# Kernel tuning notes

Measured on AMD Instinct MI355X. Metric: run time of the kernel, lower is better.

Reference implementation:

```python
import jax, jax.numpy as jnp
import numpy as np

HEAD_SIZE = 64


def setup_inputs() -> dict:
    key = jax.random.key(0)
    ks = jax.random.split(key, 6)
    B, S, D, H = 8, 2048, 1024, HEAD_SIZE
    return {
        "q": jax.random.normal(ks[0], (B, S, D), dtype=jnp.float32),
        "k": jax.random.normal(ks[1], (B, S, D), dtype=jnp.float32),
        "v": jax.random.normal(ks[2], (B, S, D), dtype=jnp.float32),
        "mask": jnp.ones((B, S), dtype=bool),
        "Wq": jax.random.normal(ks[3], (D, H), dtype=jnp.float32) * (D ** -0.5),
        "Wk": jax.random.normal(ks[4], (D, H), dtype=jnp.float32) * (D ** -0.5),
        "Wv": jax.random.normal(ks[5], (D, H), dtype=jnp.float32) * (D ** -0.5),
    }


def reference(q, k, v, mask, Wq, Wk, Wv):
    # Linear projections (bias=False): x @ W, W is [n_embd, head_size]
    qp = jnp.einsum("bsd,dh->bsh", q, Wq)
    kp = jnp.einsum("bsd,dh->bsh", k, Wk)
    vp = jnp.einsum("bsd,dh->bsh", v, Wv)
    scale = HEAD_SIZE ** -0.5
    scores = jnp.einsum("bqh,bkh->bqk", qp, kp) * scale  # [B, Sq, Sk]
    # 2-D mask [B, Sk] -> broadcast over query dim (mask.unsqueeze(1))
    scores = jnp.where(mask[:, None, :], scores, -jnp.inf)
    attn = jax.nn.softmax(scores, axis=-1)
    # dropout is identity in eval mode (deterministic reference)
    out = jnp.einsum("bqk,bkh->bqh", attn, vp)
    return out
```

## Files before the change

### kernel.cpp

```cpp
#include <hip/hip_runtime.h>
#include <hip/hip_bf16.h>
#include <math.h>

#define B_ 8
#define S_ 2048
#define D_ 1024
#define H_ 64
#define M_ (B_*S_)
#define SPLIT 4
#define KEYS_PER_SPLIT (S_/SPLIT)

typedef __attribute__((ext_vector_type(8))) short bf16x8;
typedef __attribute__((ext_vector_type(8))) unsigned short u16x8;
typedef __attribute__((ext_vector_type(4))) float f32x4;

__device__ inline unsigned short f2bf(float f) {
    unsigned int u = __builtin_bit_cast(unsigned int, f);
    u += 0x7fffu + ((u >> 16) & 1u);
    return (unsigned short)(u >> 16);
}

__global__ __launch_bounds__(256) void mask_kernel(const unsigned char* __restrict__ mask,
                                                   float* __restrict__ mmul, int n) {
    int j = blockIdx.x * 256 + threadIdx.x;
    if (j >= n) return;
    bool boolLayout = mask[1] != 0;
    int mv = boolLayout ? (int)mask[j] : ((const int*)mask)[j];
    mmul[j] = mv ? 1.0f : 0.0f;
}

__global__ __launch_bounds__(256) void wprep_kernel(
    const float* __restrict__ Wq, const float* __restrict__ Wk, const float* __restrict__ Wv,
    unsigned short* __restrict__ Wt)
{
    const int m = blockIdx.y;
    const float* W = (m == 0) ? Wq : (m == 1) ? Wk : Wv;
    unsigned short* Wo = Wt + (size_t)m * 64 * 1024;
    __shared__ unsigned short T[64][65];
    const int t = threadIdx.x;
    const int k0 = blockIdx.x * 64;
    #pragma unroll
    for (int i = 0; i < 16; i++) {
        int vi = t + i * 256;
        int kk = vi >> 6, n = vi & 63;
        T[kk][n] = f2bf(W[(size_t)(k0 + kk) * 64 + n]);
    }
    __syncthreads();
    #pragma unroll
    for (int i = 0; i < 4; i++) {
        int vi = t + i * 256;
        int n = vi >> 4, k4 = vi & 15;
        ushort4 u;
        u.x = T[k4*4+0][n]; u.y = T[k4*4+1][n]; u.z = T[k4*4+2][n]; u.w = T[k4*4+3][n];
        *(ushort4*)&Wo[(size_t)n * 1024 + k0 + k4*4] = u;
    }
}

__global__ __launch_bounds__(256) void proj_kernel(
    const float* __restrict__ q, const float* __restrict__ kx, const float* __restrict__ vx,
    const unsigned short* __restrict__ Wt,
    unsigned short* __restrict__ qp, unsigned short* __restrict__ kp, unsigned short* __restrict__ vp)
{
    const int m = blockIdx.y;
    const float* x = (m == 0) ? q : (m == 1) ? kx : vx;
    const unsigned short* Wm = Wt + (size_t)m * 64 * 1024;
    unsigned short* outp = (m == 0) ? qp : (m == 1) ? kp : vp;

    const int t = threadIdx.x;
    const int w = t >> 6, l = t & 63;
    const int lrow = l & 15, quad = l >> 4;
    const size_t arow = (size_t)(blockIdx.x * 64 + w * 16 + lrow);
    const float* xr = x + arow * D_ + quad * 8;
    const unsigned short* wb = Wm + lrow * 1024 + quad * 8;

    f32x4 acc[4] = {};
    #pragma unroll 1
    for (int ks = 0; ks < D_; ks += 128) {
        float4 xa[8];
        bf16x8 wf[4][4];
        #pragma unroll
        for (int kk = 0; kk < 4; kk++) {
            xa[2*kk]   = *(const float4*)(xr + ks + kk*32);
            xa[2*kk+1] = *(const float4*)(xr + ks + kk*32 + 4);
        }
        #pragma unroll
        for (int kk = 0; kk < 4; kk++)
            #pragma unroll
            for (int c = 0; c < 4; c++)
                wf[kk][c] = *(const bf16x8*)(wb + ks + kk*32 + c * 16 * 1024);
        __builtin_amdgcn_sched_barrier(0);
        #pragma unroll
        for (int kk = 0; kk < 4; kk++) {
            bf16x8 af;
            af[0] = (short)f2bf(xa[2*kk].x); af[1] = (short)f2bf(xa[2*kk].y);
            af[2] = (short)f2bf(xa[2*kk].z); af[3] = (short)f2bf(xa[2*kk].w);
            af[4] = (short)f2bf(xa[2*kk+1].x); af[5] = (short)f2bf(xa[2*kk+1].y);
            af[6] = (short)f2bf(xa[2*kk+1].z); af[7] = (short)f2bf(xa[2*kk+1].w);
            #pragma unroll
            for (int c = 0; c < 4; c++)
                acc[c] = __builtin_amdgcn_mfma_f32_16x16x32_bf16(af, wf[kk][c], acc[c], 0, 0, 0);
        }
    }
    const float sc = (m == 0) ? 0.125f : 1.0f;
    const int orow = blockIdx.x * 64 + w * 16 + quad * 4;
    #pragma unroll
    for (int c = 0; c < 4; c++)
        #pragma unroll
        for (int r = 0; r < 4; r++)
            outp[(size_t)(orow + r) * H_ + c * 16 + lrow] = f2bf(acc[c][r] * sc);
}

__global__ __launch_bounds__(256) void attn_kernel(
    const unsigned short* __restrict__ qp, const unsigned short* __restrict__ kp,
    const unsigned short* __restrict__ vp, const float* __restrict__ mmul,
    float* __restrict__ po, float* __restrict__ pl)
{
    __shared__ unsigned short Qs[64][72];
    __shared__ unsigned short Ks[64][72];
    __shared__ unsigned short Vt[64][72];
    __shared__ unsigned short Ps[64][72];

    const int t = threadIdx.x;
    const int w = t >> 6, l = t & 63;
    const int lrow = l & 15, lq = l >> 4;
    const int lk8 = lq * 8;
    const int b = blockIdx.y, q0 = blockIdx.x * 64;
    const int split = blockIdx.z;
    const int key0 = split * KEYS_PER_SPLIT;
    const size_t basebs = (size_t)b * S_;

    const int srow = t >> 3, sc8 = t & 7;

    #pragma unroll
    for (int i = 0; i < 2; i++) {
        u16x8 u = *(const u16x8*)&qp[(basebs + q0 + srow + i*32) * H_ + sc8 * 8];
        *(u16x8*)&Qs[srow + i*32][sc8 * 8] = u;
    }

    u16x8 kr[2], vr[2];
    #pragma unroll
    for (int i = 0; i < 2; i++) {
        kr[i] = *(const u16x8*)&kp[(basebs + key0 + srow + i*32) * H_ + sc8 * 8];
        vr[i] = *(const u16x8*)&vp[(basebs + key0 + srow + i*32) * H_ + sc8 * 8];
    }

    float lsum[4] = {0.f, 0.f, 0.f, 0.f};
    f32x4 o[4] = {};

    for (int kt = 0; kt < KEYS_PER_SPLIT / 64; kt++) {
        __syncthreads();
        #pragma unroll
        for (int i = 0; i < 2; i++) {
            *(u16x8*)&Ks[srow + i*32][sc8 * 8] = kr[i];
            #pragma unroll
            for (int j = 0; j < 8; j++)
                Vt[sc8*8 + j][(srow + i*32) ^ (sc8*8)] = vr[i][j];
        }
        __syncthreads();
        if (kt + 1 < KEYS_PER_SPLIT / 64) {
            const int k0n = key0 + (kt + 1) * 64;
            #pragma unroll
            for (int i = 0; i < 2; i++) {
                kr[i] = *(const u16x8*)&kp[(basebs + k0n + srow + i*32) * H_ + sc8 * 8];
                vr[i] = *(const u16x8*)&vp[(basebs + k0n + srow + i*32) * H_ + sc8 * 8];
            }
        }
        const int k0 = key0 + kt * 64;
        float mm[4];
        #pragma unroll
        for (int c = 0; c < 4; c++) mm[c] = mmul[basebs + k0 + c*16 + lrow];

        f32x4 s[4] = {};
        #pragma unroll
        for (int kk = 0; kk < 2; kk++) {
            bf16x8 aq = *(const bf16x8*)&Qs[w*16 + lrow][kk*32 + lk8];
            #pragma unroll
            for (int c = 0; c < 4; c++) {
                bf16x8 bk = *(const bf16x8*)&Ks[c*16 + lrow][kk*32 + lk8];
                s[c] = __builtin_amdgcn_mfma_f32_16x16x32_bf16(aq, bk, s[c], 0, 0, 0);
            }
        }
        #pragma unroll
        for (int r = 0; r < 4; r++) {
            float p0 = __expf(s[0][r]) * mm[0];
            float p1 = __expf(s[1][r]) * mm[1];
            float p2 = __expf(s[2][r]) * mm[2];
            float p3 = __expf(s[3][r]) * mm[3];
            lsum[r] += (p0 + p1) + (p2 + p3);
            const int pr = w*16 + lq*4 + r;
            Ps[pr][ 0 + lrow] = f2bf(p0);
            Ps[pr][16 + lrow] = f2bf(p1);
            Ps[pr][32 + lrow] = f2bf(p2);
            Ps[pr][48 + lrow] = f2bf(p3);
        }
        #pragma unroll
        for (int kk = 0; kk < 2; kk++) {
            bf16x8 ap = *(const bf16x8*)&Ps[w*16 + lrow][kk*32 + lk8];
            #pragma unroll
            for (int c = 0; c < 4; c++) {
                const int h = c*16 + lrow;
                const int sw = ((h >> 3) & 7) * 8;
                bf16x8 bv = *(const bf16x8*)&Vt[h][(kk*32 + lk8) ^ sw];
                o[c] = __builtin_amdgcn_mfma_f32_16x16x32_bf16(ap, bv, o[c], 0, 0, 0);
            }
        }
    }

    float* pob = po + (size_t)split * M_ * H_;
    float* plb = pl + (size_t)split * M_;
    #pragma unroll
    for (int r = 0; r < 4; r++) {
        #pragma unroll
        for (int d = 1; d < 16; d <<= 1)
            lsum[r] += __shfl_xor(lsum[r], d, 64);
        const size_t row = basebs + q0 + w*16 + lq*4 + r;
        if (lrow == 0) plb[row] = lsum[r];
        #pragma unroll
        for (int c = 0; c < 4; c++)
            pob[row * H_ + c*16 + lrow] = o[c][r];
    }
}

__global__ __launch_bounds__(256) void combine_kernel(
    const float* __restrict__ po, const float* __restrict__ pl, float* __restrict__ out)
{
    const int idx = blockIdx.x * 256 + threadIdx.x;
    const size_t row = idx >> 4;
    const int c4 = (idx & 15) * 4;
    float lt = 0.f;
    #pragma unroll
    for (int s = 0; s < SPLIT; s++) lt += pl[(size_t)s * M_ + row];
    f32x4 acc = {};
    #pragma unroll
    for (int s = 0; s < SPLIT; s++) {
        const f32x4 p = *(const f32x4*)&po[((size_t)s * M_ + row) * H_ + c4];
        acc += p;
    }
    const float inv = 1.0f / lt;
    f32x4 r = acc * inv;
    *(f32x4*)&out[row * H_ + c4] = r;
}

extern "C" void kernel_launch(void* const* d_in, const int* in_sizes, int n_in,
                              void* d_out, int out_size, void* d_ws, size_t ws_size,
                              hipStream_t stream) {
    const float* q  = (const float*)d_in[0];
    const float* k  = (const float*)d_in[1];
    const float* v  = (const float*)d_in[2];
    const unsigned char* mask = (const unsigned char*)d_in[3];
    const float* Wq = (const float*)d_in[4];
    const float* Wk = (const float*)d_in[5];
    const float* Wv = (const float*)d_in[6];
    float* out = (float*)d_out;

    unsigned short* qp = (unsigned short*)d_ws;
    unsigned short* kp = qp + (size_t)M_ * H_;
    unsigned short* vp = kp + (size_t)M_ * H_;
    float* mmul = (float*)(vp + (size_t)M_ * H_);
    unsigned short* Wt = (unsigned short*)(mmul + M_);
    float* po = (float*)(Wt + (size_t)3 * 64 * 1024);
    float* pl = po + (size_t)SPLIT * M_ * H_;

    wprep_kernel<<<dim3(16, 3), dim3(256), 0, stream>>>(Wq, Wk, Wv, Wt);
    mask_kernel<<<dim3((M_ + 255)/256), dim3(256), 0, stream>>>(mask, mmul, M_);
    proj_kernel<<<dim3(M_/64, 3), dim3(256), 0, stream>>>(q, k, v, Wt, qp, kp, vp);
    attn_kernel<<<dim3(S_/64, B_, SPLIT), dim3(256), 0, stream>>>(qp, kp, vp, mmul, po, pl);
    combine_kernel<<<dim3(M_*16/256), dim3(256), 0, stream>>>(po, pl, out);
}
```

Before: 266.5 us.

## Stage projection and attention tiles via async global-to-LDS loads, transpose V

The projection kernel now stages each 128-wide K-slice of the fp32 activations and the bf16 weights into swizzled LDS using direct global-to-LDS async loads, instead of each lane loading its fragments straight from global memory. The V projection is written transposed (per batch, head-dim major), so the attention kernel can fetch K and V tiles with async 16-byte global-to-LDS copies into XOR-swizzled buffers. This removes the per-element scalar LDS transpose of V in the attention loop. The trade-off is that the register prefetch of the next K/V tile is gone, and both kernels wait on a barrier for each tile with no double buffering. The projection kernel also uses 48KB of LDS per block, which may limit occupancy.

```diff
diff --git a/kernel.cpp b/kernel.cpp
--- a/kernel.cpp
+++ b/kernel.cpp
@@ -8,7 +8,7 @@
 #define H_ 64
 #define M_ (B_*S_)
 #define SPLIT 4
-#define KEYS_PER_SPLIT (S_/SPLIT)
+#define KPS (S_/SPLIT)
 
 typedef __attribute__((ext_vector_type(8))) short bf16x8;
 typedef __attribute__((ext_vector_type(8))) unsigned short u16x8;
@@ -18,6 +18,11 @@
     unsigned int u = __builtin_bit_cast(unsigned int, f);
     u += 0x7fffu + ((u >> 16) & 1u);
     return (unsigned short)(u >> 16);
+}
+
+__device__ inline void async16(const void* g, void* l) {
+    __builtin_amdgcn_global_load_lds((const __attribute__((address_space(1))) void*)g,
+                                     (__attribute__((address_space(3))) void*)l, 16, 0, 0);
 }
 
 __global__ __launch_bounds__(256) void mask_kernel(const unsigned char* __restrict__ mask,
@@ -59,124 +64,148 @@
 __global__ __launch_bounds__(256) void proj_kernel(
     const float* __restrict__ q, const float* __restrict__ kx, const float* __restrict__ vx,
     const unsigned short* __restrict__ Wt,
-    unsigned short* __restrict__ qp, unsigned short* __restrict__ kp, unsigned short* __restrict__ vp)
-{
+    unsigned short* __restrict__ qp, unsigned short* __restrict__ kp, unsigned short* __restrict__ vpT)
+{
+    __shared__ float          Ax[64 * 128];
+    __shared__ unsigned short Wl[64 * 128];
+
     const int m = blockIdx.y;
     const float* x = (m == 0) ? q : (m == 1) ? kx : vx;
     const unsigned short* Wm = Wt + (size_t)m * 64 * 1024;
-    unsigned short* outp = (m == 0) ? qp : (m == 1) ? kp : vp;
 
     const int t = threadIdx.x;
     const int w = t >> 6, l = t & 63;
     const int lrow = l & 15, quad = l >> 4;
-    const size_t arow = (size_t)(blockIdx.x * 64 + w * 16 + lrow);
-    const float* xr = x + arow * D_ + quad * 8;
-    const unsigned short* wb = Wm + lrow * 1024 + quad * 8;
+    const int row0 = blockIdx.x * 64;
 
     f32x4 acc[4] = {};
-    #pragma unroll 1
+
     for (int ks = 0; ks < D_; ks += 128) {
-        float4 xa[8];
-        bf16x8 wf[4][4];
+        __syncthreads();
+        #pragma unroll
+        for (int j = 0; j < 8; j++) {
+            int p = (w * 8 + j) * 64 + l;
+            int r = p >> 5;
+            int cc = (p & 31) ^ (r & 7);
+            async16(&x[(size_t)(row0 + r) * D_ + ks + cc * 4], &Ax[p * 4]);
+        }
+        #pragma unroll
+        for (int j = 0; j < 4; j++) {
+            int p = (w * 4 + j) * 64 + l;
+            int n = p >> 4;
+            int kc = (p & 15) ^ (n & 7);
+            async16(&Wm[(size_t)n * 1024 + ks + kc * 8], &Wl[p * 8]);
+        }
+        __syncthreads();
+
+        const int r = w * 16 + lrow;
         #pragma unroll
         for (int kk = 0; kk < 4; kk++) {
-            xa[2*kk]   = *(const float4*)(xr + ks + kk*32);
-            xa[2*kk+1] = *(const float4*)(xr + ks + kk*32 + 4);
-        }
-        #pragma unroll
-        for (int kk = 0; kk < 4; kk++)
+            const int c32 = kk * 8 + quad * 2;
+            f32x4 a0 = *(const f32x4*)&Ax[(r * 32 + ((c32    ) ^ (r & 7))) * 4];
+            f32x4 a1 = *(const f32x4*)&Ax[(r * 32 + ((c32 + 1) ^ (r & 7))) * 4];
+            bf16x8 af;
+            af[0] = (short)f2bf(a0.x); af[1] = (short)f2bf(a0.y);
+            af[2] = (short)f2bf(a0.z); af[3] = (short)f2bf(a0.w);
+            af[4] = (short)f2bf(a1.x); af[5] = (short)f2bf(a1.y);
+            af[6] = (short)f2bf(a1.z); af[7] = (short)f2bf(a1.w);
+            #pragma unroll
+            for (int c = 0; c < 4; c++) {
+                const int n = c * 16 + lrow;
+                bf16x8 bf = *(const bf16x8*)&Wl[(n * 16 + ((kk * 4 + quad) ^ (n & 7))) * 8];
+                acc[c] = __builtin_amdgcn_mfma_f32_16x16x32_bf16(af, bf, acc[c], 0, 0, 0);
+            }
+        }
+    }
+
+    const int orow = row0 + w * 16 + quad * 4;
+    if (m < 2) {
+        unsigned short* outp = (m == 0) ? qp : kp;
+        const float sc = (m == 0) ? 0.125f : 1.0f;
+        #pragma unroll
+        for (int c = 0; c < 4; c++)
+            #pragma unroll
+            for (int rr = 0; rr < 4; rr++)
+                outp[(size_t)(orow + rr) * H_ + c * 16 + lrow] = f2bf(acc[c][rr]);
+        if (m == 0) {
             #pragma unroll
             for (int c = 0; c < 4; c++)
-                wf[kk][c] = *(const bf16x8*)(wb + ks + kk*32 + c * 16 * 1024);
-        __builtin_amdgcn_sched_barrier(0);
-        #pragma unroll
-        for (int kk = 0; kk < 4; kk++) {
-            bf16x8 af;
-            af[0] = (short)f2bf(xa[2*kk].x); af[1] = (short)f2bf(xa[2*kk].y);
-            af[2] = (short)f2bf(xa[2*kk].z); af[3] = (short)f2bf(xa[2*kk].w);
-            af[4] = (short)f2bf(xa[2*kk+1].x); af[5] = (short)f2bf(xa[2*kk+1].y);
-            af[6] = (short)f2bf(xa[2*kk+1].z); af[7] = (short)f2bf(xa[2*kk+1].w);
-            #pragma unroll
-            for (int c = 0; c < 4; c++)
-                acc[c] = __builtin_amdgcn_mfma_f32_16x16x32_bf16(af, wf[kk][c], acc[c], 0, 0, 0);
-        }
-    }
-    const float sc = (m == 0) ? 0.125f : 1.0f;
-    const int orow = blockIdx.x * 64 + w * 16 + quad * 4;
-    #pragma unroll
-    for (int c = 0; c < 4; c++)
-        #pragma unroll
-        for (int r = 0; r < 4; r++)
-            outp[(size_t)(orow + r) * H_ + c * 16 + lrow] = f2bf(acc[c][r] * sc);
+                #pragma unroll
+                for (int rr = 0; rr < 4; rr++)
+                    outp[(size_t)(orow + rr) * H_ + c * 16 + lrow] = f2bf(acc[c][rr] * sc);
+        }
+    } else {
+        const int bb = orow >> 11;
+        const int s0 = orow & (S_ - 1);
+        #pragma unroll
+        for (int c = 0; c < 4; c++) {
+            ushort4 u;
+            u.x = f2bf(acc[c][0]); u.y = f2bf(acc[c][1]);
+            u.z = f2bf(acc[c][2]); u.w = f2bf(acc[c][3]);
+            *(ushort4*)&vpT[((size_t)bb * H_ + c * 16 + lrow) * S_ + s0] = u;
+        }
+    }
 }
 
 __global__ __launch_bounds__(256) void attn_kernel(
     const unsigned short* __restrict__ qp, const unsigned short* __restrict__ kp,
-    const unsigned short* __restrict__ vp, const float* __restrict__ mmul,
+    const unsigned short* __restrict__ vpT, const float* __restrict__ mmul,
     float* __restrict__ po, float* __restrict__ pl)
 {
     __shared__ unsigned short Qs[64][72];
-    __shared__ unsigned short Ks[64][72];
-    __shared__ unsigned short Vt[64][72];
     __shared__ unsigned short Ps[64][72];
+    __shared__ unsigned short Ks[64 * 64];
+    __shared__ unsigned short Vt[64 * 64];
 
     const int t = threadIdx.x;
     const int w = t >> 6, l = t & 63;
-    const int lrow = l & 15, lq = l >> 4;
-    const int lk8 = lq * 8;
-    const int b = blockIdx.y, q0 = blockIdx.x * 64;
-    const int split = blockIdx.z;
-    const int key0 = split * KEYS_PER_SPLIT;
+    const int lrow = l & 15, quad = l >> 4;
+    const int b = blockIdx.y, q0 = blockIdx.x * 64, split = blockIdx.z;
+    const int key0 = split * KPS;
     const size_t basebs = (size_t)b * S_;
-
-    const int srow = t >> 3, sc8 = t & 7;
+    const unsigned short* vb = vpT + (size_t)b * H_ * S_;
 
     #pragma unroll
     for (int i = 0; i < 2; i++) {
-        u16x8 u = *(const u16x8*)&qp[(basebs + q0 + srow + i*32) * H_ + sc8 * 8];
-        *(u16x8*)&Qs[srow + i*32][sc8 * 8] = u;
-    }
-
-    u16x8 kr[2], vr[2];
-    #pragma unroll
-    for (int i = 0; i < 2; i++) {
-        kr[i] = *(const u16x8*)&kp[(basebs + key0 + srow + i*32) * H_ + sc8 * 8];
-        vr[i] = *(const u16x8*)&vp[(basebs + key0 + srow + i*32) * H_ + sc8 * 8];
+        int p = t + i * 256;
+        int r = p >> 3, c8 = p & 7;
+        u16x8 u = *(const u16x8*)&qp[(basebs + q0 + r) * H_ + c8 * 8];
+        *(u16x8*)&Qs[r][c8 * 8] = u;
     }
 
     float lsum[4] = {0.f, 0.f, 0.f, 0.f};
     f32x4 o[4] = {};
 
-    for (int kt = 0; kt < KEYS_PER_SPLIT / 64; kt++) {
-        __syncthreads();
-        #pragma unroll
-        for (int i = 0; i < 2; i++) {
-            *(u16x8*)&Ks[srow + i*32][sc8 * 8] = kr[i];
-            #pragma unroll
-            for (int j = 0; j < 8; j++)
-                Vt[sc8*8 + j][(srow + i*32) ^ (sc8*8)] = vr[i][j];
-        }
-        __syncthreads();
-        if (kt + 1 < KEYS_PER_SPLIT / 64) {
-            const int k0n = key0 + (kt + 1) * 64;
-            #pragma unroll
-            for (int i = 0; i < 2; i++) {
-                kr[i] = *(const u16x8*)&kp[(basebs + k0n + srow + i*32) * H_ + sc8 * 8];
-                vr[i] = *(const u16x8*)&vp[(basebs + k0n + srow + i*32) * H_ + sc8 * 8];
-            }
-        }
+    for (int kt = 0; kt < KPS / 64; kt++) {
         const int k0 = key0 + kt * 64;
+        __syncthreads();
+        #pragma unroll
+        for (int j = 0; j < 2; j++) {
+            int p = (w * 2 + j) * 64 + l;
+            int r = p >> 3;
+            int c8 = (p & 7) ^ (r & 7);
+            async16(&kp[(basebs + k0 + r) * H_ + c8 * 8], &Ks[p * 8]);
+        }
+        #pragma unroll
+        for (int j = 0; j < 2; j++) {
+            int p = (w * 2 + j) * 64 + l;
+            int h = p >> 3;
+            int c8 = (p & 7) ^ (h & 7);
+            async16(&vb[(size_t)h * S_ + k0 + c8 * 8], &Vt[p * 8]);
+        }
         float mm[4];
         #pragma unroll
         for (int c = 0; c < 4; c++) mm[c] = mmul[basebs + k0 + c*16 + lrow];
+        __syncthreads();
 
         f32x4 s[4] = {};
         #pragma unroll
         for (int kk = 0; kk < 2; kk++) {
-            bf16x8 aq = *(const bf16x8*)&Qs[w*16 + lrow][kk*32 + lk8];
+            bf16x8 aq = *(const bf16x8*)&Qs[w*16 + lrow][kk*32 + quad*8];
             #pragma unroll
             for (int c = 0; c < 4; c++) {
-                bf16x8 bk = *(const bf16x8*)&Ks[c*16 + lrow][kk*32 + lk8];
+                const int n = c*16 + lrow;
+                bf16x8 bk = *(const bf16x8*)&Ks[(n * 8 + ((kk*4 + quad) ^ (n & 7))) * 8];
                 s[c] = __builtin_amdgcn_mfma_f32_16x16x32_bf16(aq, bk, s[c], 0, 0, 0);
             }
         }
@@ -187,7 +216,7 @@
             float p2 = __expf(s[2][r]) * mm[2];
             float p3 = __expf(s[3][r]) * mm[3];
             lsum[r] += (p0 + p1) + (p2 + p3);
-            const int pr = w*16 + lq*4 + r;
+            const int pr = w*16 + quad*4 + r;
             Ps[pr][ 0 + lrow] = f2bf(p0);
             Ps[pr][16 + lrow] = f2bf(p1);
             Ps[pr][32 + lrow] = f2bf(p2);
@@ -195,12 +224,11 @@
         }
         #pragma unroll
         for (int kk = 0; kk < 2; kk++) {
-            bf16x8 ap = *(const bf16x8*)&Ps[w*16 + lrow][kk*32 + lk8];
+            bf16x8 ap = *(const bf16x8*)&Ps[w*16 + lrow][kk*32 + quad*8];
             #pragma unroll
             for (int c = 0; c < 4; c++) {
                 const int h = c*16 + lrow;
-                const int sw = ((h >> 3) & 7) * 8;
-                bf16x8 bv = *(const bf16x8*)&Vt[h][(kk*32 + lk8) ^ sw];
+                bf16x8 bv = *(const bf16x8*)&Vt[(h * 8 + ((kk*4 + quad) ^ (h & 7))) * 8];
                 o[c] = __builtin_amdgcn_mfma_f32_16x16x32_bf16(ap, bv, o[c], 0, 0, 0);
             }
         }
@@ -213,7 +241,7 @@
         #pragma unroll
         for (int d = 1; d < 16; d <<= 1)
             lsum[r] += __shfl_xor(lsum[r], d, 64);
-        const size_t row = basebs + q0 + w*16 + lq*4 + r;
+        const size_t row = basebs + q0 + w*16 + quad*4 + r;
         if (lrow == 0) plb[row] = lsum[r];
         #pragma unroll
         for (int c = 0; c < 4; c++)
@@ -253,17 +281,17 @@
     const float* Wv = (const float*)d_in[6];
     float* out = (float*)d_out;
 
-    unsigned short* qp = (unsigned short*)d_ws;
-    unsigned short* kp = qp + (size_t)M_ * H_;
-    unsigned short* vp = kp + (size_t)M_ * H_;
-    float* mmul = (float*)(vp + (size_t)M_ * H_);
+    unsigned short* qp  = (unsigned short*)d_ws;
+    unsigned short* kp  = qp + (size_t)M_ * H_;
+    unsigned short* vpT = kp + (size_t)M_ * H_;
+    float* mmul = (float*)(vpT + (size_t)M_ * H_);
     unsigned short* Wt = (unsigned short*)(mmul + M_);
     float* po = (float*)(Wt + (size_t)3 * 64 * 1024);
     float* pl = po + (size_t)SPLIT * M_ * H_;
 
     wprep_kernel<<<dim3(16, 3), dim3(256), 0, stream>>>(Wq, Wk, Wv, Wt);
     mask_kernel<<<dim3((M_ + 255)/256), dim3(256), 0, stream>>>(mask, mmul, M_);
-    proj_kernel<<<dim3(M_/64, 3), dim3(256), 0, stream>>>(q, k, v, Wt, qp, kp, vp);
-    attn_kernel<<<dim3(S_/64, B_, SPLIT), dim3(256), 0, stream>>>(qp, kp, vp, mmul, po, pl);
+    proj_kernel<<<dim3(M_/64, 3), dim3(256), 0, stream>>>(q, k, v, Wt, qp, kp, vpT);
+    attn_kernel<<<dim3(S_/64, B_, SPLIT), dim3(256), 0, stream>>>(qp, kp, vpT, mmul, po, pl);
     combine_kernel<<<dim3(M_*16/256), dim3(256), 0, stream>>>(po, pl, out);
 }
```

New measurement: 244.3 us. 8.3% less time.
